# Performance work log

Measured on AMD Instinct MI355X. Metric: run time of the kernel, lower is better.

The kernel has to match this reference:

```python
import jax, jax.numpy as jnp
import numpy as np

N_NODES = 50000
N_EDGES = 800000
IN_DIM, H1, H2, OUT_DIM = 128, 512, 256, 1


def glorot(key, shape):
    fan_in, fan_out = shape
    lim = jnp.sqrt(6.0 / (fan_in + fan_out))
    return jax.random.uniform(key, shape, jnp.float32, -lim, lim)


def setup_inputs() -> dict:
    key = jax.random.key(0)
    ks = jax.random.split(key, 6)
    x = jax.random.normal(ks[0], (N_NODES, IN_DIM), jnp.float32)
    edge_index = jax.random.randint(ks[1], (2, N_EDGES), 0, N_NODES, jnp.int32)
    edge_attr = jax.random.uniform(ks[2], (N_EDGES,), jnp.float32)
    return {
        "x": x,
        "edge_index": edge_index,
        "edge_attr": edge_attr,
        "W1": glorot(ks[3], (IN_DIM, H1)), "b1": jnp.zeros((H1,), jnp.float32),
        "W2": glorot(ks[4], (H1, H2)), "b2": jnp.zeros((H2,), jnp.float32),
        "W3": glorot(ks[5], (H2, OUT_DIM)), "b3": jnp.zeros((OUT_DIM,), jnp.float32),
    }


def gcn_conv(x, src, dst, ew, W, b, n_nodes):
    # PyG GCNConv with edge weights, normalize=True, add_self_loops=True.
    h = x @ W                                            # [N, F_out]
    # degree includes self-loop weight 1.0 at each node
    deg = jax.ops.segment_sum(ew, dst, num_segments=n_nodes) + 1.0  # [N]
    dis = jnp.where(deg > 0, jax.lax.rsqrt(deg), 0.0)    # deg^{-1/2}
    norm = dis[src] * ew * dis[dst]                      # [E]
    msgs = h[src] * norm[:, None]                        # [E, F_out] gather
    agg = jax.ops.segment_sum(msgs, dst, num_segments=n_nodes)      # scatter-add
    # self-loop contribution: norm_ii = dis_i * 1 * dis_i = 1/deg_i
    agg = agg + h * (dis * dis)[:, None]
    return agg + b


def reference(x, edge_index, edge_attr, W1, b1, W2, b2, W3, b3):
    src, dst = edge_index[0], edge_index[1]
    n = x.shape[0]
    h = jax.nn.relu(gcn_conv(x, src, dst, edge_attr, W1, b1, n))
    h = jax.nn.relu(gcn_conv(h, src, dst, edge_attr, W2, b2, n))
    return gcn_conv(h, src, dst, edge_attr, W3, b3, n)
```

## Files before the change

kernel.cpp:

```cpp
#include <hip/hip_runtime.h>
#include <hip/hip_bf16.h>
#include <stdint.h>

typedef unsigned short u16;
typedef unsigned long long u64;
typedef __attribute__((ext_vector_type(8))) short bf16x8;
typedef __attribute__((ext_vector_type(4))) float f32x4;

constexpr int N_NODES = 50000;
constexpr int N_EDGES = 800000;
constexpr int IN_DIM  = 128;
constexpr int H1_DIM  = 512;
constexpr int H2_DIM  = 256;
constexpr int MT      = 64;
constexpr int MP      = 50048;
constexpr int CAP     = 64;
constexpr int PREP_NB = 3125;

constexpr float DEG_SCALE = 268435456.0f;
constexpr float DEG_INV   = 1.0f / 268435456.0f;

__device__ __forceinline__ u16 f2b(float f) {
  union { float f; unsigned u; } v{f};
  unsigned r = v.u + 0x7fff + ((v.u >> 16) & 1);
  return (u16)(r >> 16);
}
__device__ __forceinline__ float b2f(u16 h) {
  union { unsigned u; float f; } v;
  v.u = ((unsigned)h) << 16;
  return v.f;
}

__device__ __forceinline__ void async16(void* lds, const void* g) {
  __builtin_amdgcn_global_load_lds(
      (const __attribute__((address_space(1))) unsigned int*)g,
      (__attribute__((address_space(3))) unsigned int*)lds, 16, 0, 0);
}

__global__ __launch_bounds__(256) void prep_kernel(
    const int* __restrict__ src, const int* __restrict__ dst,
    const float* __restrict__ ew, u64* __restrict__ degcnt,
    u64* __restrict__ erec,
    const float* __restrict__ x, u16* __restrict__ xb,
    const float* __restrict__ W1, u16* __restrict__ w1t,
    const float* __restrict__ W2, u16* __restrict__ w2t) {
  int b = blockIdx.x, t = threadIdx.x;
  {
    int e = b * 256 + t;
    int d = dst[e];
    float w = ew[e];
    u64 inc = ((u64)1 << 40) | (u64)(w * DEG_SCALE + 0.5f);
    u64 old = atomicAdd(&degcnt[d], inc);
    int slot = (int)(old >> 40);
    if (slot < CAP)
      erec[(size_t)d * CAP + slot] =
          ((u64)__float_as_uint(w) << 32) | (unsigned)src[e];
  }
#pragma unroll
  for (int r = 0; r < 2; ++r) {
    int i = b * 512 + r * 256 + t;
    float4 v = *(const float4*)&x[(size_t)i * 4];
    ushort4 o;
    o.x = f2b(v.x); o.y = f2b(v.y); o.z = f2b(v.z); o.w = f2b(v.w);
    *(ushort4*)&xb[(size_t)i * 4] = o;
  }
  if (t < 21) {
    int i = b * 21 + t;
    if (i < H1_DIM * IN_DIM) {
      int nn = i / IN_DIM, k = i - nn * IN_DIM;
      w1t[i] = f2b(W1[(size_t)k * H1_DIM + nn]);
    }
  }
  if (t < 42) {
    int i = b * 42 + t;
    if (i < H2_DIM * H1_DIM) {
      int nn = i / H1_DIM, k = i - nn * H1_DIM;
      w2t[i] = f2b(W2[(size_t)k * H2_DIM + nn]);
    }
  }
}

__global__ __launch_bounds__(256) void dis_cnt_kernel(
    const u64* __restrict__ degcnt, float* __restrict__ dis,
    int* __restrict__ cnt8, int n) {
  int i = blockIdx.x * 256 + threadIdx.x;
  if (i >= n) return;
  u64 v = degcnt[i];
  int cnt = (int)(v >> 40);
  float deg = (float)(v & 0xFFFFFFFFFFULL) * DEG_INV;
  dis[i] = rsqrtf(deg + 1.0f);
  cnt8[i] = min((cnt + 7) & ~7, CAP);
}

__global__ __launch_bounds__(256) void norm_pad_kernel(
    u64* __restrict__ erec, const u64* __restrict__ degcnt,
    const int* __restrict__ cnt8, const float* __restrict__ dis) {
  int wid = threadIdx.x >> 6, lane = threadIdx.x & 63;
  int node = blockIdx.x * 4 + wid;
  int cnt = (int)(degcnt[node] >> 40);
  int c8 = cnt8[node];
  if (lane >= c8) return;
  u64* slot = erec + (size_t)node * CAP + lane;
  u64 outv = 0;
  if (lane < cnt) {
    u64 rec = *slot;
    int s = (int)(unsigned)rec;
    float w = __uint_as_float((unsigned)(rec >> 32));
    w *= dis[s] * dis[node];
    outv = ((u64)__float_as_uint(w) << 32) | (unsigned)s;
  }
  *slot = outv;
}

__global__ __launch_bounds__(256) void agg128_kernel(
    const u16* __restrict__ X, const int* __restrict__ cnt8,
    const u64* __restrict__ erec, const float* __restrict__ dis,
    u16* __restrict__ Y) {
  int wid = threadIdx.x >> 6, lane = threadIdx.x & 63;
  int node = __builtin_amdgcn_readfirstlane(blockIdx.x * 4 + wid);
  float d = dis[node];
  float dd = d * d;
  const u16* Xl = X + lane * 2;
  const u64* re = erec + (size_t)node * CAP;
  int c8 = cnt8[node];
  ushort2 sv = *(const ushort2*)(Xl + (size_t)node * 128);
  float a0 = b2f(sv.x) * dd, a1 = b2f(sv.y) * dd;
  for (int j = 0; j < c8; j += 8) {
    u64 r[8];
#pragma unroll
    for (int q = 0; q < 8; ++q) r[q] = re[j + q];
    ushort2 vv[8];
#pragma unroll
    for (int q = 0; q < 8; ++q)
      vv[q] = *(const ushort2*)(Xl + (size_t)(unsigned)(r[q] & 0xFFFFFFFFu) * 128);
#pragma unroll
    for (int q = 0; q < 8; ++q) {
      float w = __uint_as_float((unsigned)(r[q] >> 32));
      a0 += b2f(vv[q].x) * w;
      a1 += b2f(vv[q].y) * w;
    }
  }
  unsigned pk = ((unsigned)f2b(a1) << 16) | (unsigned)f2b(a0);
  *(unsigned*)(Y + (size_t)node * 128 + lane * 2) = pk;
}

__global__ __launch_bounds__(256) void agg256_gemv_kernel(
    const u16* __restrict__ X, const int* __restrict__ cnt8,
    const u64* __restrict__ erec, const float* __restrict__ dis,
    const float* __restrict__ b2, const float* __restrict__ W3,
    float* __restrict__ T) {
  int wid = threadIdx.x >> 6, lane = threadIdx.x & 63;
  int node = __builtin_amdgcn_readfirstlane(blockIdx.x * 4 + wid);
  float d = dis[node];
  float dd = d * d;
  const u16* Xl = X + lane * 4;
  const u64* re = erec + (size_t)node * CAP;
  int c8 = cnt8[node];
  ushort4 sv = *(const ushort4*)(Xl + (size_t)node * 256);
  float a0 = b2f(sv.x) * dd, a1 = b2f(sv.y) * dd;
  float a2 = b2f(sv.z) * dd, a3 = b2f(sv.w) * dd;
  for (int j = 0; j < c8; j += 8) {
    u64 r[8];
#pragma unroll
    for (int q = 0; q < 8; ++q) r[q] = re[j + q];
    ushort4 vv[8];
#pragma unroll
    for (int q = 0; q < 8; ++q)
      vv[q] = *(const ushort4*)(Xl + (size_t)(unsigned)(r[q] & 0xFFFFFFFFu) * 256);
#pragma unroll
    for (int q = 0; q < 8; ++q) {
      float w = __uint_as_float((unsigned)(r[q] >> 32));
      a0 += b2f(vv[q].x) * w;
      a1 += b2f(vv[q].y) * w;
      a2 += b2f(vv[q].z) * w;
      a3 += b2f(vv[q].w) * w;
    }
  }
  float4 bv = *(const float4*)&b2[lane * 4];
  float4 wv = *(const float4*)&W3[lane * 4];
  float s = fmaxf(a0 + bv.x, 0.f) * wv.x + fmaxf(a1 + bv.y, 0.f) * wv.y +
            fmaxf(a2 + bv.z, 0.f) * wv.z + fmaxf(a3 + bv.w, 0.f) * wv.w;
#pragma unroll
  for (int off = 32; off; off >>= 1) s += __shfl_down(s, off);
  if (lane == 0) T[node] = s;
}

__global__ __launch_bounds__(512, 4) void fused_gemm_kernel(
    const u16* __restrict__ xa, const u16* __restrict__ w1t,
    const u16* __restrict__ w2t, const float* __restrict__ b1,
    u16* __restrict__ t2b, int Mstore) {
  __shared__ u16 xa_s[MT * 128];
  __shared__ u16 h1_s[MT * 128];
  __shared__ u16 ws_s[256 * 64];
  int tid = threadIdx.x;
  int m0 = blockIdx.x * MT;
  int lane = tid & 63, w = tid >> 6;
  int l15 = lane & 15, l4 = lane >> 4;
  int wa = w >> 1;
  int wb = w & 1;

  {
    const char* xb = (const char*)xa + (size_t)m0 * 256;
#pragma unroll
    for (int i = 0; i < 2; ++i) {
      int L = i * 8192 + tid * 16;
      int row = L >> 8;
      int srcoff = (row << 8) + ((L & 255) ^ ((row & 7) << 4));
      async16((char*)xa_s + i * 8192 + (tid & ~63) * 16, xb + srcoff);
    }
  }

  f32x4 acc2[4][2];
#pragma unroll
  for (int i = 0; i < 4; ++i)
#pragma unroll
    for (int j = 0; j < 2; ++j) acc2[i][j] = (f32x4){0.f, 0.f, 0.f, 0.f};

  for (int c = 0; c < 4; ++c) {
    f32x4 acc1[2][2];
#pragma unroll
    for (int i = 0; i < 2; ++i)
#pragma unroll
      for (int j = 0; j < 2; ++j) acc1[i][j] = (f32x4){0.f, 0.f, 0.f, 0.f};

#pragma unroll
    for (int ko = 0; ko < 2; ++ko) {
      {
        const char* wsrc = (const char*)w1t + (size_t)(c * 128) * 256 + ko * 128;
#pragma unroll
        for (int i = 0; i < 2; ++i) {
          int L = i * 8192 + tid * 16;
          int row = L >> 7;
          int srcoff = (row << 8) + ((L & 127) ^ ((row & 7) << 4));
          async16((char*)ws_s + i * 8192 + (tid & ~63) * 16, wsrc + srcoff);
        }
      }
      __syncthreads();
#pragma unroll
      for (int ki = 0; ki < 2; ++ki) {
        bf16x8 a1[2], bx[2];
#pragma unroll
        for (int fn = 0; fn < 2; ++fn) {
          int nr = wa * 32 + fn * 16 + l15;
          int byte = (nr * 128 + ki * 64 + l4 * 16) ^ ((nr & 7) << 4);
          a1[fn] = *(const bf16x8*)((const char*)ws_s + byte);
        }
#pragma unroll
        for (int fm = 0; fm < 2; ++fm) {
          int mr = wb * 32 + fm * 16 + l15;
          int byte = (mr * 256 + ko * 128 + ki * 64 + l4 * 16) ^ ((mr & 7) << 4);
          bx[fm] = *(const bf16x8*)((const char*)xa_s + byte);
        }
#pragma unroll
        for (int fn = 0; fn < 2; ++fn)
#pragma unroll
          for (int fm = 0; fm < 2; ++fm)
            acc1[fn][fm] = __builtin_amdgcn_mfma_f32_16x16x32_bf16(
                a1[fn], bx[fm], acc1[fn][fm], 0, 0, 0);
      }
      __syncthreads();
    }

#pragma unroll
    for (int fn = 0; fn < 2; ++fn) {
      int nloc = wa * 32 + fn * 16 + l4 * 4;
      float4 bv = *(const float4*)&b1[c * 128 + nloc];
#pragma unroll
      for (int fm = 0; fm < 2; ++fm) {
        int mr = wb * 32 + fm * 16 + l15;
        u16 p0 = f2b(fmaxf(acc1[fn][fm][0] + bv.x, 0.f));
        u16 p1 = f2b(fmaxf(acc1[fn][fm][1] + bv.y, 0.f));
        u16 p2 = f2b(fmaxf(acc1[fn][fm][2] + bv.z, 0.f));
        u16 p3 = f2b(fmaxf(acc1[fn][fm][3] + bv.w, 0.f));
        u64 pk = ((u64)p3 << 48) | ((u64)p2 << 32) | ((u64)p1 << 16) | p0;
        int byte = (mr * 256 + nloc * 2) ^ ((mr & 7) << 4);
        *(u64*)((char*)h1_s + byte) = pk;
      }
    }
    __syncthreads();

#pragma unroll
    for (int ko = 0; ko < 2; ++ko) {
      {
        const char* wsrc = (const char*)w2t + (size_t)(c * 128 + ko * 64) * 2;
#pragma unroll
        for (int i = 0; i < 4; ++i) {
          int L = i * 8192 + tid * 16;
          int row = L >> 7;
          int srcoff = row * 1024 + ((L & 127) ^ ((row & 7) << 4));
          async16((char*)ws_s + i * 8192 + (tid & ~63) * 16, wsrc + srcoff);
        }
      }
      __syncthreads();
#pragma unroll
      for (int ki = 0; ki < 2; ++ki) {
        bf16x8 a2[4], bh[2];
#pragma unroll
        for (int fnn = 0; fnn < 4; ++fnn) {
          int nr = wa * 64 + fnn * 16 + l15;
          int byte = (nr * 128 + ki * 64 + l4 * 16) ^ ((nr & 7) << 4);
          a2[fnn] = *(const bf16x8*)((const char*)ws_s + byte);
        }
#pragma unroll
        for (int fm = 0; fm < 2; ++fm) {
          int mr = wb * 32 + fm * 16 + l15;
          int byte = (mr * 256 + ko * 128 + ki * 64 + l4 * 16) ^ ((mr & 7) << 4);
          bh[fm] = *(const bf16x8*)((const char*)h1_s + byte);
        }
#pragma unroll
        for (int fnn = 0; fnn < 4; ++fnn)
#pragma unroll
          for (int fm = 0; fm < 2; ++fm)
            acc2[fnn][fm] = __builtin_amdgcn_mfma_f32_16x16x32_bf16(
                a2[fnn], bh[fm], acc2[fnn][fm], 0, 0, 0);
      }
      __syncthreads();
    }
  }

#pragma unroll
  for (int fnn = 0; fnn < 4; ++fnn) {
    int nn = wa * 64 + fnn * 16 + l4 * 4;
#pragma unroll
    for (int fm = 0; fm < 2; ++fm) {
      int m = m0 + wb * 32 + fm * 16 + l15;
      if (m < Mstore) {
        ushort4 pk;
        pk.x = f2b(acc2[fnn][fm][0]);
        pk.y = f2b(acc2[fnn][fm][1]);
        pk.z = f2b(acc2[fnn][fm][2]);
        pk.w = f2b(acc2[fnn][fm][3]);
        *(ushort4*)(t2b + (size_t)m * 256 + nn) = pk;
      }
    }
  }
}

__global__ __launch_bounds__(256) void agg_out_kernel(
    const float* __restrict__ T, const int* __restrict__ cnt8,
    const u64* __restrict__ erec, const float* __restrict__ dis,
    const float* __restrict__ b3, float* __restrict__ out, int n) {
  const int4* E4 = (const int4*)erec;
  int i = blockIdx.x * 256 + threadIdx.x;
  if (i >= n) return;
  float d = dis[i];
  float acc = T[i] * d * d;
  int c8 = cnt8[i];
  int h0 = i * (CAP / 2);
  for (int e = 0; e < c8; e += 8) {
    int h = h0 + (e >> 1);
    int4 r0 = E4[h], r1 = E4[h + 1], r2 = E4[h + 2], r3 = E4[h + 3];
    acc += T[r0.x] * __int_as_float(r0.y) + T[r0.z] * __int_as_float(r0.w) +
           T[r1.x] * __int_as_float(r1.y) + T[r1.z] * __int_as_float(r1.w) +
           T[r2.x] * __int_as_float(r2.y) + T[r2.z] * __int_as_float(r2.w) +
           T[r3.x] * __int_as_float(r3.y) + T[r3.z] * __int_as_float(r3.w);
  }
  out[i] = acc + b3[0];
}

extern "C" void kernel_launch(void* const* d_in, const int* in_sizes, int n_in,
                              void* d_out, int out_size, void* d_ws, size_t ws_size,
                              hipStream_t stream) {
  const float* x  = (const float*)d_in[0];
  const int*   ei = (const int*)d_in[1];
  const float* ew = (const float*)d_in[2];
  const float* W1 = (const float*)d_in[3];
  const float* b1 = (const float*)d_in[4];
  const float* W2 = (const float*)d_in[5];
  const float* b2 = (const float*)d_in[6];
  const float* W3 = (const float*)d_in[7];
  const float* b3 = (const float*)d_in[8];
  float* out = (float*)d_out;

  const int N = N_NODES, E = N_EDGES;
  const int* src = ei;
  const int* dst = ei + E;

  char* p = (char*)d_ws;
  auto alloc = [&](size_t bytes) -> char* {
    char* r = p;
    p += (bytes + 255) & ~(size_t)255;
    return r;
  };
  u64*   degcnt  = (u64*)  alloc((size_t)N * 8);
  float* dis     = (float*)alloc((size_t)N * 4);
  int*   cnt8    = (int*)  alloc((size_t)N * 4);
  u64*   erec    = (u64*)  alloc((size_t)N * CAP * 8);
  u16*   w1t     = (u16*)  alloc((size_t)H1_DIM * IN_DIM * 2);
  u16*   w2t     = (u16*)  alloc((size_t)H2_DIM * H1_DIM * 2);
  u16*   xb      = (u16*)  alloc((size_t)N * IN_DIM * 2);
  u16*   xa      = (u16*)  alloc((size_t)MP * IN_DIM * 2);
  u16*   t2b     = (u16*)  alloc((size_t)N * H2_DIM * 2);
  float* t3      = (float*)alloc((size_t)N * 4);

  hipMemsetAsync(degcnt, 0, (size_t)N * 8, stream);
  hipMemsetAsync(xa + (size_t)N * IN_DIM, 0, (size_t)(MP - N) * IN_DIM * 2, stream);

  prep_kernel<<<PREP_NB, 256, 0, stream>>>(src, dst, ew, degcnt, erec,
                                           x, xb, W1, w1t, W2, w2t);

  dis_cnt_kernel<<<(N + 255) / 256, 256, 0, stream>>>(degcnt, dis, cnt8, N);
  norm_pad_kernel<<<N / 4, 256, 0, stream>>>(erec, degcnt, cnt8, dis);

  agg128_kernel<<<N / 4, 256, 0, stream>>>(xb, cnt8, erec, dis, xa);

  fused_gemm_kernel<<<MP / MT, 512, 0, stream>>>(xa, w1t, w2t, b1, t2b, N);

  agg256_gemv_kernel<<<N / 4, 256, 0, stream>>>(t2b, cnt8, erec, dis, b2, W3, t3);

  agg_out_kernel<<<(N + 255) / 256, 256, 0, stream>>>(t3, cnt8, erec, dis,
                                                      b3, out, N);
}
```

Baseline: 200.6 us.

## Shard degree atomics four ways and compact staged edge lists, unroll gathers by 16

The per-destination atomic counter is split into four shards chosen by thread index, which spreads contention across more addresses. Each shard writes into its own staging region, and a new compact kernel merges the shards, normalizes the weights and pads each list to a multiple of 16. The aggregation kernels now unroll their gather loops by 16 instead of 8. The cost is an extra staging buffer plus another read and write pass over it, more zero padding per node, and more registers in the aggregation loops. Per-shard capacity is capped at 24, so a node whose edges pile into one shard could drop edges.

```diff
diff --git a/kernel.cpp b/kernel.cpp
--- a/kernel.cpp
+++ b/kernel.cpp
@@ -15,6 +15,9 @@
 constexpr int MT      = 64;
 constexpr int MP      = 50048;
 constexpr int CAP     = 64;
+constexpr int NSH     = 4;
+constexpr int RSH     = 24;
+constexpr int SCAP    = NSH * RSH;
 constexpr int PREP_NB = 3125;
 
 constexpr float DEG_SCALE = 268435456.0f;
@@ -39,8 +42,8 @@
 
 __global__ __launch_bounds__(256) void prep_kernel(
     const int* __restrict__ src, const int* __restrict__ dst,
-    const float* __restrict__ ew, u64* __restrict__ degcnt,
-    u64* __restrict__ erec,
+    const float* __restrict__ ew, u64* __restrict__ degsh,
+    u64* __restrict__ stage,
     const float* __restrict__ x, u16* __restrict__ xb,
     const float* __restrict__ W1, u16* __restrict__ w1t,
     const float* __restrict__ W2, u16* __restrict__ w2t) {
@@ -49,11 +52,12 @@
     int e = b * 256 + t;
     int d = dst[e];
     float w = ew[e];
+    int sh = t & 3;
     u64 inc = ((u64)1 << 40) | (u64)(w * DEG_SCALE + 0.5f);
-    u64 old = atomicAdd(&degcnt[d], inc);
+    u64 old = atomicAdd(&degsh[(size_t)sh * N_NODES + d], inc);
     int slot = (int)(old >> 40);
-    if (slot < CAP)
-      erec[(size_t)d * CAP + slot] =
+    if (slot < RSH)
+      stage[(size_t)d * SCAP + sh * RSH + slot] =
           ((u64)__float_as_uint(w) << 32) | (unsigned)src[e];
   }
 #pragma unroll
@@ -81,35 +85,44 @@
 }
 
 __global__ __launch_bounds__(256) void dis_cnt_kernel(
-    const u64* __restrict__ degcnt, float* __restrict__ dis,
-    int* __restrict__ cnt8, int n) {
+    const u64* __restrict__ degsh, float* __restrict__ dis, int n) {
   int i = blockIdx.x * 256 + threadIdx.x;
   if (i >= n) return;
-  u64 v = degcnt[i];
-  int cnt = (int)(v >> 40);
+  u64 v = degsh[i] + degsh[(size_t)n + i] + degsh[(size_t)2 * n + i] +
+          degsh[(size_t)3 * n + i];
   float deg = (float)(v & 0xFFFFFFFFFFULL) * DEG_INV;
   dis[i] = rsqrtf(deg + 1.0f);
-  cnt8[i] = min((cnt + 7) & ~7, CAP);
-}
-
-__global__ __launch_bounds__(256) void norm_pad_kernel(
-    u64* __restrict__ erec, const u64* __restrict__ degcnt,
-    const int* __restrict__ cnt8, const float* __restrict__ dis) {
+}
+
+__global__ __launch_bounds__(256) void compact_norm_kernel(
+    const u64* __restrict__ stage, const u64* __restrict__ degsh,
+    const float* __restrict__ dis, u64* __restrict__ erec,
+    int* __restrict__ cnt8, int n) {
   int wid = threadIdx.x >> 6, lane = threadIdx.x & 63;
   int node = blockIdx.x * 4 + wid;
-  int cnt = (int)(degcnt[node] >> 40);
-  int c8 = cnt8[node];
-  if (lane >= c8) return;
-  u64* slot = erec + (size_t)node * CAP + lane;
-  u64 outv = 0;
-  if (lane < cnt) {
-    u64 rec = *slot;
-    int s = (int)(unsigned)rec;
-    float w = __uint_as_float((unsigned)(rec >> 32));
-    w *= dis[s] * dis[node];
-    outv = ((u64)__float_as_uint(w) << 32) | (unsigned)s;
-  }
-  *slot = outv;
+  int c[NSH], base[NSH];
+  int tot = 0;
+#pragma unroll
+  for (int s = 0; s < NSH; ++s) {
+    c[s] = min((int)(degsh[(size_t)s * n + node] >> 40), RSH);
+    base[s] = tot;
+    tot += c[s];
+  }
+  int c16 = min((tot + 15) & ~15, CAP);
+  float dn = dis[node];
+  const u64* st = stage + (size_t)node * SCAP;
+  u64* fin = erec + (size_t)node * CAP;
+#pragma unroll
+  for (int s = 0; s < NSH; ++s) {
+    if (lane < c[s]) {
+      u64 rec = st[s * RSH + lane];
+      int sv = (int)(unsigned)rec;
+      float w = __uint_as_float((unsigned)(rec >> 32)) * dis[sv] * dn;
+      fin[base[s] + lane] = ((u64)__float_as_uint(w) << 32) | (unsigned)sv;
+    }
+  }
+  if (lane >= tot && lane < c16) fin[lane] = 0;
+  if (lane == 0) cnt8[node] = c16;
 }
 
 __global__ __launch_bounds__(256) void agg128_kernel(
@@ -122,19 +135,19 @@
   float dd = d * d;
   const u16* Xl = X + lane * 2;
   const u64* re = erec + (size_t)node * CAP;
-  int c8 = cnt8[node];
+  int c16 = cnt8[node];
   ushort2 sv = *(const ushort2*)(Xl + (size_t)node * 128);
   float a0 = b2f(sv.x) * dd, a1 = b2f(sv.y) * dd;
-  for (int j = 0; j < c8; j += 8) {
-    u64 r[8];
-#pragma unroll
-    for (int q = 0; q < 8; ++q) r[q] = re[j + q];
-    ushort2 vv[8];
-#pragma unroll
-    for (int q = 0; q < 8; ++q)
+  for (int j = 0; j < c16; j += 16) {
+    u64 r[16];
+#pragma unroll
+    for (int q = 0; q < 16; ++q) r[q] = re[j + q];
+    ushort2 vv[16];
+#pragma unroll
+    for (int q = 0; q < 16; ++q)
       vv[q] = *(const ushort2*)(Xl + (size_t)(unsigned)(r[q] & 0xFFFFFFFFu) * 128);
 #pragma unroll
-    for (int q = 0; q < 8; ++q) {
+    for (int q = 0; q < 16; ++q) {
       float w = __uint_as_float((unsigned)(r[q] >> 32));
       a0 += b2f(vv[q].x) * w;
       a1 += b2f(vv[q].y) * w;
@@ -155,20 +168,20 @@
   float dd = d * d;
   const u16* Xl = X + lane * 4;
   const u64* re = erec + (size_t)node * CAP;
-  int c8 = cnt8[node];
+  int c16 = cnt8[node];
   ushort4 sv = *(const ushort4*)(Xl + (size_t)node * 256);
   float a0 = b2f(sv.x) * dd, a1 = b2f(sv.y) * dd;
   float a2 = b2f(sv.z) * dd, a3 = b2f(sv.w) * dd;
-  for (int j = 0; j < c8; j += 8) {
-    u64 r[8];
-#pragma unroll
-    for (int q = 0; q < 8; ++q) r[q] = re[j + q];
-    ushort4 vv[8];
-#pragma unroll
-    for (int q = 0; q < 8; ++q)
+  for (int j = 0; j < c16; j += 16) {
+    u64 r[16];
+#pragma unroll
+    for (int q = 0; q < 16; ++q) r[q] = re[j + q];
+    ushort4 vv[16];
+#pragma unroll
+    for (int q = 0; q < 16; ++q)
       vv[q] = *(const ushort4*)(Xl + (size_t)(unsigned)(r[q] & 0xFFFFFFFFu) * 256);
 #pragma unroll
-    for (int q = 0; q < 8; ++q) {
+    for (int q = 0; q < 16; ++q) {
       float w = __uint_as_float((unsigned)(r[q] >> 32));
       a0 += b2f(vv[q].x) * w;
       a1 += b2f(vv[q].y) * w;
@@ -345,9 +358,9 @@
   if (i >= n) return;
   float d = dis[i];
   float acc = T[i] * d * d;
-  int c8 = cnt8[i];
+  int c16 = cnt8[i];
   int h0 = i * (CAP / 2);
-  for (int e = 0; e < c8; e += 8) {
+  for (int e = 0; e < c16; e += 8) {
     int h = h0 + (e >> 1);
     int4 r0 = E4[h], r1 = E4[h + 1], r2 = E4[h + 2], r3 = E4[h + 3];
     acc += T[r0.x] * __int_as_float(r0.y) + T[r0.z] * __int_as_float(r0.w) +
@@ -382,9 +395,10 @@
     p += (bytes + 255) & ~(size_t)255;
     return r;
   };
-  u64*   degcnt  = (u64*)  alloc((size_t)N * 8);
+  u64*   degsh   = (u64*)  alloc((size_t)NSH * N * 8);
   float* dis     = (float*)alloc((size_t)N * 4);
   int*   cnt8    = (int*)  alloc((size_t)N * 4);
+  u64*   stage   = (u64*)  alloc((size_t)N * SCAP * 8);
   u64*   erec    = (u64*)  alloc((size_t)N * CAP * 8);
   u16*   w1t     = (u16*)  alloc((size_t)H1_DIM * IN_DIM * 2);
   u16*   w2t     = (u16*)  alloc((size_t)H2_DIM * H1_DIM * 2);
@@ -393,14 +407,15 @@
   u16*   t2b     = (u16*)  alloc((size_t)N * H2_DIM * 2);
   float* t3      = (float*)alloc((size_t)N * 4);
 
-  hipMemsetAsync(degcnt, 0, (size_t)N * 8, stream);
+  hipMemsetAsync(degsh, 0, (size_t)NSH * N * 8, stream);
   hipMemsetAsync(xa + (size_t)N * IN_DIM, 0, (size_t)(MP - N) * IN_DIM * 2, stream);
 
-  prep_kernel<<<PREP_NB, 256, 0, stream>>>(src, dst, ew, degcnt, erec,
+  prep_kernel<<<PREP_NB, 256, 0, stream>>>(src, dst, ew, degsh, stage,
                                            x, xb, W1, w1t, W2, w2t);
 
-  dis_cnt_kernel<<<(N + 255) / 256, 256, 0, stream>>>(degcnt, dis, cnt8, N);
-  norm_pad_kernel<<<N / 4, 256, 0, stream>>>(erec, degcnt, cnt8, dis);
+  dis_cnt_kernel<<<(N + 255) / 256, 256, 0, stream>>>(degsh, dis, N);
+  compact_norm_kernel<<<N / 4, 256, 0, stream>>>(stage, degsh, dis, erec,
+                                                 cnt8, N);
 
   agg128_kernel<<<N / 4, 256, 0, stream>>>(xb, cnt8, erec, dis, xa);
 
```

After: 216.3 us. 1.08x slower.

## Fold symmetric degree normalization into node features and drop edge-norm pass

Applied to the files above, without the earlier changes.

The D^-1/2 A D^-1/2 normalization is split into a per-node pre-scale of source features and a post-scale of each destination result, so edge records keep their raw weights. This removes the norm_pad kernel, which rewrote every edge record and did random gathers of dis. The degree finalization, padding and x-to-bf16 conversion are merged into one finalize kernel, and the weight transposes move into the edge prep kernel. In exchange, the GEMM epilogue, the GEMV and the output kernel each do extra per-node multiplies, and bf16 rounding now happens on pre-scaled values.

```diff
diff --git a/kernel.cpp b/kernel.cpp
--- a/kernel.cpp
+++ b/kernel.cpp
@@ -41,75 +41,57 @@
     const int* __restrict__ src, const int* __restrict__ dst,
     const float* __restrict__ ew, u64* __restrict__ degcnt,
     u64* __restrict__ erec,
-    const float* __restrict__ x, u16* __restrict__ xb,
     const float* __restrict__ W1, u16* __restrict__ w1t,
     const float* __restrict__ W2, u16* __restrict__ w2t) {
-  int b = blockIdx.x, t = threadIdx.x;
-  {
-    int e = b * 256 + t;
-    int d = dst[e];
-    float w = ew[e];
-    u64 inc = ((u64)1 << 40) | (u64)(w * DEG_SCALE + 0.5f);
-    u64 old = atomicAdd(&degcnt[d], inc);
-    int slot = (int)(old >> 40);
-    if (slot < CAP)
-      erec[(size_t)d * CAP + slot] =
-          ((u64)__float_as_uint(w) << 32) | (unsigned)src[e];
-  }
-#pragma unroll
-  for (int r = 0; r < 2; ++r) {
-    int i = b * 512 + r * 256 + t;
-    float4 v = *(const float4*)&x[(size_t)i * 4];
+  int e = blockIdx.x * 256 + threadIdx.x;
+  int d = dst[e];
+  int s = src[e];
+  float w = ew[e];
+  u64 old = atomicAdd(&degcnt[d],
+                      ((u64)1 << 40) | (u64)(w * DEG_SCALE + 0.5f));
+  if (e < H1_DIM * IN_DIM) {
+    int nn = e / IN_DIM, k = e - nn * IN_DIM;
+    w1t[e] = f2b(W1[(size_t)k * H1_DIM + nn]);
+  }
+  if (e < H2_DIM * H1_DIM) {
+    int nn = e / H1_DIM, k = e - nn * H1_DIM;
+    w2t[e] = f2b(W2[(size_t)k * H2_DIM + nn]);
+  }
+  int slot = (int)(old >> 40);
+  if (slot < CAP)
+    erec[(size_t)d * CAP + slot] =
+        ((u64)__float_as_uint(w) << 32) | (unsigned)s;
+}
+
+__global__ __launch_bounds__(256) void finalize_kernel(
+    const u64* __restrict__ degcnt, float* __restrict__ dis,
+    int* __restrict__ cnt8, u64* __restrict__ erec,
+    const float* __restrict__ x, u16* __restrict__ xb) {
+  int t = blockIdx.x * 256 + threadIdx.x;
+  int row = t >> 2;
+  if (row >= N_NODES) return;
+  u64 v = degcnt[row];
+  float deg = (float)(v & 0xFFFFFFFFFFULL) * DEG_INV;
+  float dr = rsqrtf(deg + 1.0f);
+  int q = t & 3;
+  if (q == 0) {
+    dis[row] = dr;
+    int cnt = (int)(v >> 40);
+    int c8 = min((cnt + 7) & ~7, CAP);
+    cnt8[row] = c8;
+    u64* fin = erec + (size_t)row * CAP;
+    for (int j = cnt; j < c8; ++j) fin[j] = 0;
+  }
+  const float* xr = x + (size_t)row * IN_DIM + q * 32;
+  u16* xbr = xb + (size_t)row * IN_DIM + q * 32;
+#pragma unroll
+  for (int k = 0; k < 8; ++k) {
+    float4 vx = *(const float4*)(xr + k * 4);
     ushort4 o;
-    o.x = f2b(v.x); o.y = f2b(v.y); o.z = f2b(v.z); o.w = f2b(v.w);
-    *(ushort4*)&xb[(size_t)i * 4] = o;
-  }
-  if (t < 21) {
-    int i = b * 21 + t;
-    if (i < H1_DIM * IN_DIM) {
-      int nn = i / IN_DIM, k = i - nn * IN_DIM;
-      w1t[i] = f2b(W1[(size_t)k * H1_DIM + nn]);
-    }
-  }
-  if (t < 42) {
-    int i = b * 42 + t;
-    if (i < H2_DIM * H1_DIM) {
-      int nn = i / H1_DIM, k = i - nn * H1_DIM;
-      w2t[i] = f2b(W2[(size_t)k * H2_DIM + nn]);
-    }
-  }
-}
-
-__global__ __launch_bounds__(256) void dis_cnt_kernel(
-    const u64* __restrict__ degcnt, float* __restrict__ dis,
-    int* __restrict__ cnt8, int n) {
-  int i = blockIdx.x * 256 + threadIdx.x;
-  if (i >= n) return;
-  u64 v = degcnt[i];
-  int cnt = (int)(v >> 40);
-  float deg = (float)(v & 0xFFFFFFFFFFULL) * DEG_INV;
-  dis[i] = rsqrtf(deg + 1.0f);
-  cnt8[i] = min((cnt + 7) & ~7, CAP);
-}
-
-__global__ __launch_bounds__(256) void norm_pad_kernel(
-    u64* __restrict__ erec, const u64* __restrict__ degcnt,
-    const int* __restrict__ cnt8, const float* __restrict__ dis) {
-  int wid = threadIdx.x >> 6, lane = threadIdx.x & 63;
-  int node = blockIdx.x * 4 + wid;
-  int cnt = (int)(degcnt[node] >> 40);
-  int c8 = cnt8[node];
-  if (lane >= c8) return;
-  u64* slot = erec + (size_t)node * CAP + lane;
-  u64 outv = 0;
-  if (lane < cnt) {
-    u64 rec = *slot;
-    int s = (int)(unsigned)rec;
-    float w = __uint_as_float((unsigned)(rec >> 32));
-    w *= dis[s] * dis[node];
-    outv = ((u64)__float_as_uint(w) << 32) | (unsigned)s;
-  }
-  *slot = outv;
+    o.x = f2b(vx.x * dr); o.y = f2b(vx.y * dr);
+    o.z = f2b(vx.z * dr); o.w = f2b(vx.w * dr);
+    *(ushort4*)(xbr + k * 4) = o;
+  }
 }
 
 __global__ __launch_bounds__(256) void agg128_kernel(
@@ -118,13 +100,12 @@
     u16* __restrict__ Y) {
   int wid = threadIdx.x >> 6, lane = threadIdx.x & 63;
   int node = __builtin_amdgcn_readfirstlane(blockIdx.x * 4 + wid);
-  float d = dis[node];
-  float dd = d * d;
+  float dn = dis[node];
   const u16* Xl = X + lane * 2;
   const u64* re = erec + (size_t)node * CAP;
   int c8 = cnt8[node];
   ushort2 sv = *(const ushort2*)(Xl + (size_t)node * 128);
-  float a0 = b2f(sv.x) * dd, a1 = b2f(sv.y) * dd;
+  float a0 = b2f(sv.x), a1 = b2f(sv.y);
   for (int j = 0; j < c8; j += 8) {
     u64 r[8];
 #pragma unroll
@@ -140,7 +121,7 @@
       a1 += b2f(vv[q].y) * w;
     }
   }
-  unsigned pk = ((unsigned)f2b(a1) << 16) | (unsigned)f2b(a0);
+  unsigned pk = ((unsigned)f2b(a1 * dn) << 16) | (unsigned)f2b(a0 * dn);
   *(unsigned*)(Y + (size_t)node * 128 + lane * 2) = pk;
 }
 
@@ -148,17 +129,16 @@
     const u16* __restrict__ X, const int* __restrict__ cnt8,
     const u64* __restrict__ erec, const float* __restrict__ dis,
     const float* __restrict__ b2, const float* __restrict__ W3,
-    float* __restrict__ T) {
+    float* __restrict__ T2) {
   int wid = threadIdx.x >> 6, lane = threadIdx.x & 63;
   int node = __builtin_amdgcn_readfirstlane(blockIdx.x * 4 + wid);
-  float d = dis[node];
-  float dd = d * d;
+  float dn = dis[node];
   const u16* Xl = X + lane * 4;
   const u64* re = erec + (size_t)node * CAP;
   int c8 = cnt8[node];
   ushort4 sv = *(const ushort4*)(Xl + (size_t)node * 256);
-  float a0 = b2f(sv.x) * dd, a1 = b2f(sv.y) * dd;
-  float a2 = b2f(sv.z) * dd, a3 = b2f(sv.w) * dd;
+  float a0 = b2f(sv.x), a1 = b2f(sv.y);
+  float a2 = b2f(sv.z), a3 = b2f(sv.w);
   for (int j = 0; j < c8; j += 8) {
     u64 r[8];
 #pragma unroll
@@ -178,17 +158,17 @@
   }
   float4 bv = *(const float4*)&b2[lane * 4];
   float4 wv = *(const float4*)&W3[lane * 4];
-  float s = fmaxf(a0 + bv.x, 0.f) * wv.x + fmaxf(a1 + bv.y, 0.f) * wv.y +
-            fmaxf(a2 + bv.z, 0.f) * wv.z + fmaxf(a3 + bv.w, 0.f) * wv.w;
+  float s = fmaxf(a0 * dn + bv.x, 0.f) * wv.x + fmaxf(a1 * dn + bv.y, 0.f) * wv.y +
+            fmaxf(a2 * dn + bv.z, 0.f) * wv.z + fmaxf(a3 * dn + bv.w, 0.f) * wv.w;
 #pragma unroll
   for (int off = 32; off; off >>= 1) s += __shfl_down(s, off);
-  if (lane == 0) T[node] = s;
+  if (lane == 0) T2[node] = s * dn;
 }
 
 __global__ __launch_bounds__(512, 4) void fused_gemm_kernel(
     const u16* __restrict__ xa, const u16* __restrict__ w1t,
     const u16* __restrict__ w2t, const float* __restrict__ b1,
-    u16* __restrict__ t2b, int Mstore) {
+    const float* __restrict__ dis, u16* __restrict__ t2b, int Mstore) {
   __shared__ u16 xa_s[MT * 128];
   __shared__ u16 h1_s[MT * 128];
   __shared__ u16 ws_s[256 * 64];
@@ -325,11 +305,12 @@
     for (int fm = 0; fm < 2; ++fm) {
       int m = m0 + wb * 32 + fm * 16 + l15;
       if (m < Mstore) {
+        float dm = dis[m];
         ushort4 pk;
-        pk.x = f2b(acc2[fnn][fm][0]);
-        pk.y = f2b(acc2[fnn][fm][1]);
-        pk.z = f2b(acc2[fnn][fm][2]);
-        pk.w = f2b(acc2[fnn][fm][3]);
+        pk.x = f2b(acc2[fnn][fm][0] * dm);
+        pk.y = f2b(acc2[fnn][fm][1] * dm);
+        pk.z = f2b(acc2[fnn][fm][2] * dm);
+        pk.w = f2b(acc2[fnn][fm][3] * dm);
         *(ushort4*)(t2b + (size_t)m * 256 + nn) = pk;
       }
     }
@@ -337,25 +318,24 @@
 }
 
 __global__ __launch_bounds__(256) void agg_out_kernel(
-    const float* __restrict__ T, const int* __restrict__ cnt8,
+    const float* __restrict__ T2, const int* __restrict__ cnt8,
     const u64* __restrict__ erec, const float* __restrict__ dis,
     const float* __restrict__ b3, float* __restrict__ out, int n) {
   const int4* E4 = (const int4*)erec;
   int i = blockIdx.x * 256 + threadIdx.x;
   if (i >= n) return;
-  float d = dis[i];
-  float acc = T[i] * d * d;
+  float acc = T2[i];
   int c8 = cnt8[i];
   int h0 = i * (CAP / 2);
   for (int e = 0; e < c8; e += 8) {
     int h = h0 + (e >> 1);
     int4 r0 = E4[h], r1 = E4[h + 1], r2 = E4[h + 2], r3 = E4[h + 3];
-    acc += T[r0.x] * __int_as_float(r0.y) + T[r0.z] * __int_as_float(r0.w) +
-           T[r1.x] * __int_as_float(r1.y) + T[r1.z] * __int_as_float(r1.w) +
-           T[r2.x] * __int_as_float(r2.y) + T[r2.z] * __int_as_float(r2.w) +
-           T[r3.x] * __int_as_float(r3.y) + T[r3.z] * __int_as_float(r3.w);
-  }
-  out[i] = acc + b3[0];
+    acc += T2[r0.x] * __int_as_float(r0.y) + T2[r0.z] * __int_as_float(r0.w) +
+           T2[r1.x] * __int_as_float(r1.y) + T2[r1.z] * __int_as_float(r1.w) +
+           T2[r2.x] * __int_as_float(r2.y) + T2[r2.z] * __int_as_float(r2.w) +
+           T2[r3.x] * __int_as_float(r3.y) + T2[r3.z] * __int_as_float(r3.w);
+  }
+  out[i] = acc * dis[i] + b3[0];
 }
 
 extern "C" void kernel_launch(void* const* d_in, const int* in_sizes, int n_in,
@@ -397,14 +377,14 @@
   hipMemsetAsync(xa + (size_t)N * IN_DIM, 0, (size_t)(MP - N) * IN_DIM * 2, stream);
 
   prep_kernel<<<PREP_NB, 256, 0, stream>>>(src, dst, ew, degcnt, erec,
-                                           x, xb, W1, w1t, W2, w2t);
-
-  dis_cnt_kernel<<<(N + 255) / 256, 256, 0, stream>>>(degcnt, dis, cnt8, N);
-  norm_pad_kernel<<<N / 4, 256, 0, stream>>>(erec, degcnt, cnt8, dis);
+                                           W1, w1t, W2, w2t);
+
+  finalize_kernel<<<(N * 4 + 255) / 256, 256, 0, stream>>>(
+      degcnt, dis, cnt8, erec, x, xb);
 
   agg128_kernel<<<N / 4, 256, 0, stream>>>(xb, cnt8, erec, dis, xa);
 
-  fused_gemm_kernel<<<MP / MT, 512, 0, stream>>>(xa, w1t, w2t, b1, t2b, N);
+  fused_gemm_kernel<<<MP / MT, 512, 0, stream>>>(xa, w1t, w2t, b1, dis, t2b, N);
 
   agg256_gemv_kernel<<<N / 4, 256, 0, stream>>>(t2b, cnt8, erec, dis, b2, W3, t3);
 
```

After: 206.1 us. +2.7%, slower.
